# Kernel optimization log

Hardware: AMD Instinct MI355X
Metric: run time of the kernel (lower is better)

Reference implementation:

```python
import jax, jax.numpy as jnp
import numpy as np

N_NODES = 100000
N_EDGES = 1600000
IN_CH = 128
HIDDEN = 64
N_CLASSES = 40


def setup_inputs() -> dict:
    key = jax.random.key(0)
    k_x, k_e, k_w1, k_w2 = jax.random.split(key, 4)
    x = jax.random.normal(k_x, (N_NODES, IN_CH), dtype=jnp.float32)
    edge_index = jax.random.randint(k_e, (2, N_EDGES), 0, N_NODES, dtype=jnp.int64)
    # Glorot-style init for GCN weights
    W1 = jax.random.normal(k_w1, (IN_CH, HIDDEN), dtype=jnp.float32) * (1.0 / np.sqrt(IN_CH))
    b1 = jnp.zeros((HIDDEN,), dtype=jnp.float32)
    W2 = jax.random.normal(k_w2, (HIDDEN, N_CLASSES), dtype=jnp.float32) * (1.0 / np.sqrt(HIDDEN))
    b2 = jnp.zeros((N_CLASSES,), dtype=jnp.float32)
    return {"x": x, "edge_index": edge_index, "W1": W1, "b1": b1, "W2": W2, "b2": b2}


def reference(x, edge_index, W1, b1, W2, b2):
    n = x.shape[0]
    # PyG GCNConv: add self-loops, symmetric degree normalization
    loop = jnp.arange(n, dtype=edge_index.dtype)
    src = jnp.concatenate([edge_index[0], loop])  # message sources j
    dst = jnp.concatenate([edge_index[1], loop])  # aggregation targets i
    w = jnp.ones(src.shape[0], dtype=x.dtype)     # edge_weight=None -> ones
    deg = jax.ops.segment_sum(w, dst, num_segments=n)
    dinv = jnp.where(deg > 0, jax.lax.rsqrt(jnp.maximum(deg, 1e-12)), 0.0)
    norm = dinv[src] * dinv[dst]                  # [E+N]

    def gcn_conv(h, W, b):
        hw = h @ W                                # transform first (fewer flops)
        msg = hw[src] * norm[:, None]             # gather + normalize
        return jax.ops.segment_sum(msg, dst, num_segments=n) + b  # scatter-add

    h = jax.nn.relu(gcn_conv(x, W1, b1))
    # dropout is identity in eval mode
    out = gcn_conv(h, W2, b2)
    return out
```

## Files before the change

kernel.cpp:

```cpp
#include <hip/hip_runtime.h>
#include <hip/hip_bf16.h>

#define NNODES 100000
#define NEDGES 1600000
#define IN_CH 128
#define HID 64
#define NC 40
#define NPAD 100352
#define NBUK 196
#define CAP 9216
#define BCHUNK 4096
#define NBIN 391

typedef unsigned short ushort_t;
typedef unsigned int uint_t;
typedef __attribute__((ext_vector_type(8))) short short8;
typedef __attribute__((ext_vector_type(4))) float floatx4;

__device__ __forceinline__ ushort_t f2bf(float f) {
    union { float ff; unsigned int i; } t;
    t.ff = f;
    unsigned int r = t.i + 0x7fff + ((t.i >> 16) & 1);
    return (ushort_t)(r >> 16);
}
__device__ __forceinline__ float2 unpk(uint_t p) {
    union { unsigned int i; float f; } a, b;
    a.i = p << 16;
    b.i = p & 0xffff0000u;
    return make_float2(a.f, b.f);
}
__device__ __forceinline__ void acc2(float2& a, uint_t p) {
    union { unsigned int i; float f; } lo, hi;
    lo.i = p << 16;
    hi.i = p & 0xffff0000u;
    a.x += lo.f;
    a.y += hi.f;
}

__global__ __launch_bounds__(256) void k_init(
    const float* __restrict__ W1, ushort_t* __restrict__ Wp,
    int* __restrict__ gcur, ushort_t* __restrict__ hb, int n)
{
    int b = blockIdx.x, t = threadIdx.x;
    if (b < 32) {
        int i = b * 256 + t;
        int j = i & 7;
        int m = (i >> 3) & 15;
        int ct = (i >> 7) & 3;
        int quad = (i >> 9) & 3;
        int kc = i >> 11;
        int k = kc * 32 + quad * 8 + j;
        int c = ct * 16 + m;
        Wp[i] = f2bf(W1[k * HID + c]);
    } else {
        if (t < NBUK) gcur[t] = t * CAP;
        uint_t* hbz = (uint_t*)(hb + (size_t)n * HID);
        if (t >= 224) hbz[t - 224] = 0;
    }
}

__global__ __launch_bounds__(256) void k_bin0(
    const int* __restrict__ srcs, const int* __restrict__ dsts,
    int* __restrict__ gcur, uint_t* __restrict__ tmp, int e)
{
    __shared__ uint_t pk[BCHUNK];
    __shared__ ushort_t bk[BCHUNK];
    __shared__ int hist[NBUK];
    __shared__ int base[NBUK];
    int t = threadIdx.x;
    int begin = blockIdx.x * BCHUNK;
    int cnt = e - begin; if (cnt > BCHUNK) cnt = BCHUNK;

    for (int i = t; i < NBUK; i += 256) hist[i] = 0;
    __syncthreads();
    for (int j = t; j < cnt; j += 256) {
        int d = dsts[begin + j];
        int s = srcs[begin + j];
        int b = d >> 9;
        pk[j] = (uint_t)s | ((uint_t)(d & 511) << 17);
        bk[j] = (ushort_t)b;
        atomicAdd(&hist[b], 1);
    }
    __syncthreads();
    for (int i = t; i < NBUK; i += 256) {
        base[i] = atomicAdd(&gcur[i], hist[i]);
        hist[i] = 0;
    }
    __syncthreads();
    for (int j = t; j < cnt; j += 256) {
        int b = bk[j];
        int r = atomicAdd(&hist[b], 1);
        int pos = base[b] + r;
        if (pos < (b + 1) * CAP) tmp[pos] = pk[j];
    }
}

__global__ __launch_bounds__(256) void k_sort(
    const uint_t* __restrict__ tmp, const int* __restrict__ gcur,
    int* __restrict__ row_start, float* __restrict__ dinv,
    uint_t* __restrict__ es, int n, int e)
{
    __shared__ int cnt[512];
    __shared__ int sc[512];
    __shared__ int red[256];
    int t = threadIdx.x;
    int b = blockIdx.x;
    int d0 = b << 9;
    int total = gcur[b] - b * CAP;
    if (total > CAP) total = CAP;
    int part = 0;
    for (int i = t; i < b; i += 256) part += gcur[i] - i * CAP;
    red[t] = part;
    cnt[t] = 0; cnt[t + 256] = 0;
    __syncthreads();
    for (int off = 128; off > 0; off >>= 1) {
        if (t < off) red[t] += red[t + off];
        __syncthreads();
    }
    int gb = red[0];
    const uint_t* seg = tmp + b * CAP;
    for (int j = t; j < total; j += 256)
        atomicAdd(&cnt[seg[j] >> 17], 1);
    __syncthreads();
    sc[t] = cnt[t]; sc[t + 256] = cnt[t + 256];
    __syncthreads();
    for (int off = 1; off < 512; off <<= 1) {
        int v0 = (t >= off) ? sc[t - off] : 0;
        int i1 = t + 256;
        int v1 = (i1 >= off) ? sc[i1 - off] : 0;
        __syncthreads();
        sc[t] += v0; sc[i1] += v1;
        __syncthreads();
    }
#pragma unroll
    for (int q = 0; q < 2; ++q) {
        int i = t + q * 256;
        int node = d0 + i;
        int start = gb + sc[i] - cnt[i];
        if (node < n) {
            row_start[node] = start;
            dinv[node] = rsqrtf((float)cnt[i] + 1.0f);
        }
        cnt[i] = start;
    }
    __syncthreads();
    for (int j = t; j < total; j += 256) {
        uint_t p = seg[j];
        int ld = (int)(p >> 17);
        int pos = atomicAdd(&cnt[ld], 1);
        es[pos] = p & 0x1FFFFu;
    }
    if (b == NBUK - 1 && t == 0) row_start[n] = e;
}

__global__ __launch_bounds__(256) void k_gemm1(
    const float* __restrict__ x, const ushort_t* __restrict__ Wp,
    const float* __restrict__ dinv, ushort_t* __restrict__ hw1, int n)
{
    int wave = threadIdx.x >> 6;
    int lane = threadIdx.x & 63;
    int m = lane & 15;
    int quad = lane >> 4;
    int row = blockIdx.x * 64 + wave * 16 + m;
    int rowc = row < n ? row : (n - 1);
    const float* xr = x + (size_t)rowc * IN_CH + quad * 8;

    floatx4 acc[4];
#pragma unroll
    for (int ct = 0; ct < 4; ++ct) acc[ct] = (floatx4){0.f, 0.f, 0.f, 0.f};

#pragma unroll
    for (int kc = 0; kc < 4; ++kc) {
        float4 xa = *(const float4*)(xr + kc * 32);
        float4 xb = *(const float4*)(xr + kc * 32 + 4);
        short8 a;
        a[0] = (short)f2bf(xa.x); a[1] = (short)f2bf(xa.y);
        a[2] = (short)f2bf(xa.z); a[3] = (short)f2bf(xa.w);
        a[4] = (short)f2bf(xb.x); a[5] = (short)f2bf(xb.y);
        a[6] = (short)f2bf(xb.z); a[7] = (short)f2bf(xb.w);
#pragma unroll
        for (int ct = 0; ct < 4; ++ct) {
            short8 b = *(const short8*)(Wp + ((((kc * 4 + quad) * 4 + ct) * 16 + m) << 3));
            acc[ct] = __builtin_amdgcn_mfma_f32_16x16x32_bf16(a, b, acc[ct], 0, 0, 0);
        }
    }
    int r0 = blockIdx.x * 64 + wave * 16 + quad * 4;
#pragma unroll
    for (int r = 0; r < 4; ++r) {
        int rr = r0 + r;
        if (rr < n) {
            float di = dinv[rr];
            ushort_t* o = hw1 + (size_t)rr * HID + m;
#pragma unroll
            for (int ct = 0; ct < 4; ++ct) o[ct * 16] = f2bf(acc[ct][r] * di);
        } else if (rr == n) {
            ushort_t* o = hw1 + (size_t)n * HID + m;
#pragma unroll
            for (int ct = 0; ct < 4; ++ct) o[ct * 16] = 0;
        }
    }
}

__global__ __launch_bounds__(256) void k_agg1(
    const int* __restrict__ row_start, const uint_t* __restrict__ es,
    const float* __restrict__ dinv, const uint_t* __restrict__ hw1u,
    const float* __restrict__ b1, ushort_t* __restrict__ hb, int n)
{
    int lane = threadIdx.x & 63;
    int obase = lane & 56;
    int ol = lane & 7;
    int node = blockIdx.x * 32 + (threadIdx.x >> 3);
    bool valid = node < n;
    int rs = valid ? row_start[node] : 0;
    int re = valid ? row_start[node + 1] : 0;
    float di = valid ? dinv[node] : 0.f;
    int selfrow = valid ? node : n;

    float2 c0, c1, c2, c3;
    {
        uint4 sp = *(const uint4*)(hw1u + (size_t)selfrow * 32 + ol * 4);
        c0 = unpk(sp.x); c1 = unpk(sp.y); c2 = unpk(sp.z); c3 = unpk(sp.w);
    }
    for (int base = rs; base < re; base += 8) {
        int idx = base + ol;
        int el = (idx < re) ? (int)es[idx] : n;
        uint4 p[8];
#pragma unroll
        for (int b = 0; b < 8; ++b) {
            int s = __shfl(el, obase + b);
            p[b] = *(const uint4*)(hw1u + (size_t)s * 32 + ol * 4);
        }
#pragma unroll
        for (int b = 0; b < 8; ++b) {
            acc2(c0, p[b].x); acc2(c1, p[b].y);
            acc2(c2, p[b].z); acc2(c3, p[b].w);
        }
    }
    if (valid) {
        float4 bb0 = ((const float4*)b1)[ol * 2];
        float4 bb1 = ((const float4*)b1)[ol * 2 + 1];
        float h0 = fmaxf(c0.x * di + bb0.x, 0.f);
        float h1 = fmaxf(c0.y * di + bb0.y, 0.f);
        float h2 = fmaxf(c1.x * di + bb0.z, 0.f);
        float h3 = fmaxf(c1.y * di + bb0.w, 0.f);
        float h4 = fmaxf(c2.x * di + bb1.x, 0.f);
        float h5 = fmaxf(c2.y * di + bb1.y, 0.f);
        float h6 = fmaxf(c3.x * di + bb1.z, 0.f);
        float h7 = fmaxf(c3.y * di + bb1.w, 0.f);
        uint4 st;
        st.x = (uint_t)f2bf(h0 * di) | ((uint_t)f2bf(h1 * di) << 16);
        st.y = (uint_t)f2bf(h2 * di) | ((uint_t)f2bf(h3 * di) << 16);
        st.z = (uint_t)f2bf(h4 * di) | ((uint_t)f2bf(h5 * di) << 16);
        st.w = (uint_t)f2bf(h6 * di) | ((uint_t)f2bf(h7 * di) << 16);
        *(uint4*)(hb + (size_t)node * HID + ol * 8) = st;
    }
}

__global__ __launch_bounds__(256) void k_agg2(
    const int* __restrict__ row_start, const uint_t* __restrict__ es,
    const float* __restrict__ dinv, const uint_t* __restrict__ hbu,
    float* __restrict__ hagg, int n)
{
    int lane = threadIdx.x & 63;
    int obase = lane & 56;
    int ol = lane & 7;
    int node = blockIdx.x * 32 + (threadIdx.x >> 3);
    bool valid = node < n;
    int rs = valid ? row_start[node] : 0;
    int re = valid ? row_start[node + 1] : 0;
    float di = valid ? dinv[node] : 0.f;
    int selfrow = valid ? node : n;

    float2 c0, c1, c2, c3;
    {
        uint4 sp = *(const uint4*)(hbu + (size_t)selfrow * 32 + ol * 4);
        c0 = unpk(sp.x); c1 = unpk(sp.y); c2 = unpk(sp.z); c3 = unpk(sp.w);
    }
    for (int base = rs; base < re; base += 8) {
        int idx = base + ol;
        int el = (idx < re) ? (int)es[idx] : n;
        uint4 p[8];
#pragma unroll
        for (int b = 0; b < 8; ++b) {
            int s = __shfl(el, obase + b);
            p[b] = *(const uint4*)(hbu + (size_t)s * 32 + ol * 4);
        }
#pragma unroll
        for (int b = 0; b < 8; ++b) {
            acc2(c0, p[b].x); acc2(c1, p[b].y);
            acc2(c2, p[b].z); acc2(c3, p[b].w);
        }
    }
    if (valid) {
        float4 o0, o1;
        o0.x = c0.x * di; o0.y = c0.y * di; o0.z = c1.x * di; o0.w = c1.y * di;
        o1.x = c2.x * di; o1.y = c2.y * di; o1.z = c3.x * di; o1.w = c3.y * di;
        float* hr = hagg + (size_t)node * HID + ol * 8;
        *(float4*)hr = o0;
        *(float4*)(hr + 4) = o1;
    }
}

__global__ __launch_bounds__(256) void k_gemm2f(
    const float* __restrict__ hagg, const float* __restrict__ W2,
    const float* __restrict__ b2, float* __restrict__ out, int n)
{
    __shared__ float wsm[HID * NC];
    for (int i = threadIdx.x; i < HID * NC; i += 256) wsm[i] = W2[i];
    __syncthreads();
    int row = blockIdx.x * 256 + threadIdx.x;
    if (row >= n) return;
    const float4* hr = (const float4*)(hagg + (size_t)row * HID);
    float acc[NC];
#pragma unroll
    for (int c = 0; c < NC; ++c) acc[c] = b2[c];
#pragma unroll 4
    for (int k4 = 0; k4 < HID / 4; ++k4) {
        float4 hv = hr[k4];
        const float* w0 = wsm + (k4 * 4) * NC;
#pragma unroll
        for (int c = 0; c < NC; ++c)
            acc[c] += hv.x * w0[c] + hv.y * w0[c + NC] + hv.z * w0[c + 2 * NC] + hv.w * w0[c + 3 * NC];
    }
    float* o = out + (size_t)row * NC;
#pragma unroll
    for (int c4 = 0; c4 < NC / 4; ++c4) {
        float4 st = make_float4(acc[4 * c4], acc[4 * c4 + 1], acc[4 * c4 + 2], acc[4 * c4 + 3]);
        *(float4*)(o + 4 * c4) = st;
    }
}

extern "C" void kernel_launch(void* const* d_in, const int* in_sizes, int n_in,
                              void* d_out, int out_size, void* d_ws, size_t ws_size,
                              hipStream_t stream) {
    const float* x  = (const float*)d_in[0];
    const int* edge = (const int*)d_in[1];
    const float* W1 = (const float*)d_in[2];
    const float* b1 = (const float*)d_in[3];
    const float* W2 = (const float*)d_in[4];
    const float* b2 = (const float*)d_in[5];
    float* out      = (float*)d_out;

    const int n = in_sizes[0] / IN_CH;
    const int e = in_sizes[1] / 2;
    const int* srcs = edge;
    const int* dsts = edge + e;

    int*      gcur      = (int*)d_ws;
    int*      row_start = gcur + 256;
    float*    dinv      = (float*)(row_start + NPAD);
    uint_t*   tmp       = (uint_t*)(dinv + NPAD);
    uint_t*   es        = tmp + (size_t)NBUK * CAP;
    ushort_t* Wp        = (ushort_t*)(es + NEDGES);
    ushort_t* hw1       = Wp + 8192;
    ushort_t* hb        = hw1 + (size_t)(NNODES + 1) * HID;
    float*    hagg      = (float*)(hb + (size_t)(NNODES + 1) * HID);

    k_init<<<33, 256, 0, stream>>>(W1, Wp, gcur, hb, n);
    k_bin0<<<NBIN, 256, 0, stream>>>(srcs, dsts, gcur, tmp, e);
    k_sort<<<NBUK, 256, 0, stream>>>(tmp, gcur, row_start, dinv, es, n, e);
    k_gemm1<<<(n + 63) / 64, 256, 0, stream>>>(x, Wp, dinv, hw1, n);
    k_agg1<<<(n + 31) / 32, 256, 0, stream>>>(row_start, es, dinv, (const uint_t*)hw1, b1, hb, n);
    k_agg2<<<(n + 31) / 32, 256, 0, stream>>>(row_start, es, dinv, (const uint_t*)hb, hagg, n);
    k_gemm2f<<<(n + 255) / 256, 256, 0, stream>>>(hagg, W2, b2, out, n);
}
```

Before: 238.1 us.

## Fuse second GEMM into layer-2 aggregation and fold init into binning kernel

The layer-2 aggregation now keeps each block's 32 aggregated rows in shared memory and multiplies them by W2 (staged in LDS) directly, writing the final output. This removes the fp32 hagg intermediate round trip through global memory and one kernel launch. The init kernel is replaced by a memset of the bucket cursors plus an extra block in the binning kernel that packs W1 and zeroes the pad row. Bucket offsets are now added at use time. Accumulators switch to a 2-wide float vector type, which may allow packed adds. Each agg2 block now does extra LDS work and holds more shared memory, which may reduce occupancy.

```diff
diff --git a/kernel.cpp b/kernel.cpp
--- a/kernel.cpp
+++ b/kernel.cpp
@@ -16,6 +16,7 @@
 typedef unsigned int uint_t;
 typedef __attribute__((ext_vector_type(8))) short short8;
 typedef __attribute__((ext_vector_type(4))) float floatx4;
+typedef __attribute__((ext_vector_type(2))) float f32x2;
 
 __device__ __forceinline__ ushort_t f2bf(float f) {
     union { float ff; unsigned int i; } t;
@@ -23,51 +24,40 @@
     unsigned int r = t.i + 0x7fff + ((t.i >> 16) & 1);
     return (ushort_t)(r >> 16);
 }
-__device__ __forceinline__ float2 unpk(uint_t p) {
-    union { unsigned int i; float f; } a, b;
-    a.i = p << 16;
-    b.i = p & 0xffff0000u;
-    return make_float2(a.f, b.f);
-}
-__device__ __forceinline__ void acc2(float2& a, uint_t p) {
+__device__ __forceinline__ void acc2(f32x2& a, uint_t p) {
     union { unsigned int i; float f; } lo, hi;
     lo.i = p << 16;
     hi.i = p & 0xffff0000u;
-    a.x += lo.f;
-    a.y += hi.f;
-}
-
-__global__ __launch_bounds__(256) void k_init(
-    const float* __restrict__ W1, ushort_t* __restrict__ Wp,
-    int* __restrict__ gcur, ushort_t* __restrict__ hb, int n)
-{
-    int b = blockIdx.x, t = threadIdx.x;
-    if (b < 32) {
-        int i = b * 256 + t;
-        int j = i & 7;
-        int m = (i >> 3) & 15;
-        int ct = (i >> 7) & 3;
-        int quad = (i >> 9) & 3;
-        int kc = i >> 11;
-        int k = kc * 32 + quad * 8 + j;
-        int c = ct * 16 + m;
-        Wp[i] = f2bf(W1[k * HID + c]);
-    } else {
-        if (t < NBUK) gcur[t] = t * CAP;
-        uint_t* hbz = (uint_t*)(hb + (size_t)n * HID);
-        if (t >= 224) hbz[t - 224] = 0;
-    }
+    f32x2 v = {lo.f, hi.f};
+    a += v;
 }
 
 __global__ __launch_bounds__(256) void k_bin0(
     const int* __restrict__ srcs, const int* __restrict__ dsts,
-    int* __restrict__ gcur, uint_t* __restrict__ tmp, int e)
+    int* __restrict__ gcur, uint_t* __restrict__ tmp, int e,
+    const float* __restrict__ W1, ushort_t* __restrict__ Wp,
+    ushort_t* __restrict__ hb, int n)
 {
     __shared__ uint_t pk[BCHUNK];
     __shared__ ushort_t bk[BCHUNK];
     __shared__ int hist[NBUK];
     __shared__ int base[NBUK];
     int t = threadIdx.x;
+    if (blockIdx.x >= NBIN) {
+        for (int i = t; i < IN_CH * HID; i += 256) {
+            int j = i & 7;
+            int m = (i >> 3) & 15;
+            int ct = (i >> 7) & 3;
+            int quad = (i >> 9) & 3;
+            int kc = i >> 11;
+            int k = kc * 32 + quad * 8 + j;
+            int c = ct * 16 + m;
+            Wp[i] = f2bf(W1[k * HID + c]);
+        }
+        uint_t* hbz = (uint_t*)(hb + (size_t)n * HID);
+        if (t < 32) hbz[t] = 0;
+        return;
+    }
     int begin = blockIdx.x * BCHUNK;
     int cnt = e - begin; if (cnt > BCHUNK) cnt = BCHUNK;
 
@@ -83,7 +73,7 @@
     }
     __syncthreads();
     for (int i = t; i < NBUK; i += 256) {
-        base[i] = atomicAdd(&gcur[i], hist[i]);
+        base[i] = i * CAP + atomicAdd(&gcur[i], hist[i]);
         hist[i] = 0;
     }
     __syncthreads();
@@ -106,10 +96,10 @@
     int t = threadIdx.x;
     int b = blockIdx.x;
     int d0 = b << 9;
-    int total = gcur[b] - b * CAP;
+    int total = gcur[b];
     if (total > CAP) total = CAP;
     int part = 0;
-    for (int i = t; i < b; i += 256) part += gcur[i] - i * CAP;
+    for (int i = t; i < b; i += 256) part += gcur[i];
     red[t] = part;
     cnt[t] = 0; cnt[t + 256] = 0;
     __syncthreads();
@@ -216,10 +206,11 @@
     float di = valid ? dinv[node] : 0.f;
     int selfrow = valid ? node : n;
 
-    float2 c0, c1, c2, c3;
+    f32x2 c0, c1, c2, c3;
     {
         uint4 sp = *(const uint4*)(hw1u + (size_t)selfrow * 32 + ol * 4);
-        c0 = unpk(sp.x); c1 = unpk(sp.y); c2 = unpk(sp.z); c3 = unpk(sp.w);
+        c0 = (f32x2){0.f, 0.f}; c1 = c0; c2 = c0; c3 = c0;
+        acc2(c0, sp.x); acc2(c1, sp.y); acc2(c2, sp.z); acc2(c3, sp.w);
     }
     for (int base = rs; base < re; base += 8) {
         int idx = base + ol;
@@ -259,22 +250,30 @@
 __global__ __launch_bounds__(256) void k_agg2(
     const int* __restrict__ row_start, const uint_t* __restrict__ es,
     const float* __restrict__ dinv, const uint_t* __restrict__ hbu,
-    float* __restrict__ hagg, int n)
-{
+    const float* __restrict__ W2, const float* __restrict__ b2,
+    float* __restrict__ out, int n)
+{
+    __shared__ float wsm[HID * NC];
+    __shared__ float hsm[32][68];
+    for (int i = threadIdx.x; i < HID * NC; i += 256) wsm[i] = W2[i];
+    __syncthreads();
+
     int lane = threadIdx.x & 63;
     int obase = lane & 56;
     int ol = lane & 7;
-    int node = blockIdx.x * 32 + (threadIdx.x >> 3);
+    int slot = threadIdx.x >> 3;
+    int node = blockIdx.x * 32 + slot;
     bool valid = node < n;
     int rs = valid ? row_start[node] : 0;
     int re = valid ? row_start[node + 1] : 0;
     float di = valid ? dinv[node] : 0.f;
     int selfrow = valid ? node : n;
 
-    float2 c0, c1, c2, c3;
+    f32x2 c0, c1, c2, c3;
     {
         uint4 sp = *(const uint4*)(hbu + (size_t)selfrow * 32 + ol * 4);
-        c0 = unpk(sp.x); c1 = unpk(sp.y); c2 = unpk(sp.z); c3 = unpk(sp.w);
+        c0 = (f32x2){0.f, 0.f}; c1 = c0; c2 = c0; c3 = c0;
+        acc2(c0, sp.x); acc2(c1, sp.y); acc2(c2, sp.z); acc2(c3, sp.w);
     }
     for (int base = rs; base < re; base += 8) {
         int idx = base + ol;
@@ -291,42 +290,37 @@
             acc2(c2, p[b].z); acc2(c3, p[b].w);
         }
     }
-    if (valid) {
-        float4 o0, o1;
-        o0.x = c0.x * di; o0.y = c0.y * di; o0.z = c1.x * di; o0.w = c1.y * di;
-        o1.x = c2.x * di; o1.y = c2.y * di; o1.z = c3.x * di; o1.w = c3.y * di;
-        float* hr = hagg + (size_t)node * HID + ol * 8;
-        *(float4*)hr = o0;
-        *(float4*)(hr + 4) = o1;
-    }
-}
-
-__global__ __launch_bounds__(256) void k_gemm2f(
-    const float* __restrict__ hagg, const float* __restrict__ W2,
-    const float* __restrict__ b2, float* __restrict__ out, int n)
-{
-    __shared__ float wsm[HID * NC];
-    for (int i = threadIdx.x; i < HID * NC; i += 256) wsm[i] = W2[i];
-    __syncthreads();
-    int row = blockIdx.x * 256 + threadIdx.x;
-    if (row >= n) return;
-    const float4* hr = (const float4*)(hagg + (size_t)row * HID);
-    float acc[NC];
-#pragma unroll
-    for (int c = 0; c < NC; ++c) acc[c] = b2[c];
+    {
+        float4 g0, g1;
+        g0.x = c0.x * di; g0.y = c0.y * di; g0.z = c1.x * di; g0.w = c1.y * di;
+        g1.x = c2.x * di; g1.y = c2.y * di; g1.z = c3.x * di; g1.w = c3.y * di;
+        *(float4*)&hsm[slot][ol * 8] = g0;
+        *(float4*)&hsm[slot][ol * 8 + 4] = g1;
+    }
+    int w8 = (threadIdx.x >> 6) * 8;
+    int qm = lane >> 4;
+    int lq = lane & 15;
+    int lw = (lq < 10) ? lq : 0;
+    const float4* w4 = (const float4*)wsm;
+#pragma unroll
+    for (int pass = 0; pass < 2; ++pass) {
+        int slot2 = w8 + pass * 4 + qm;
+        int node2 = blockIdx.x * 32 + slot2;
+        float4 acc = ((const float4*)b2)[lw];
 #pragma unroll 4
-    for (int k4 = 0; k4 < HID / 4; ++k4) {
-        float4 hv = hr[k4];
-        const float* w0 = wsm + (k4 * 4) * NC;
-#pragma unroll
-        for (int c = 0; c < NC; ++c)
-            acc[c] += hv.x * w0[c] + hv.y * w0[c + NC] + hv.z * w0[c + 2 * NC] + hv.w * w0[c + 3 * NC];
-    }
-    float* o = out + (size_t)row * NC;
-#pragma unroll
-    for (int c4 = 0; c4 < NC / 4; ++c4) {
-        float4 st = make_float4(acc[4 * c4], acc[4 * c4 + 1], acc[4 * c4 + 2], acc[4 * c4 + 3]);
-        *(float4*)(o + 4 * c4) = st;
+        for (int k4 = 0; k4 < 16; ++k4) {
+            float4 hk = *(const float4*)&hsm[slot2][k4 * 4];
+            float4 w0 = w4[(k4 * 4 + 0) * 10 + lw];
+            float4 w1 = w4[(k4 * 4 + 1) * 10 + lw];
+            float4 w2 = w4[(k4 * 4 + 2) * 10 + lw];
+            float4 w3 = w4[(k4 * 4 + 3) * 10 + lw];
+            acc.x += hk.x * w0.x + hk.y * w1.x + hk.z * w2.x + hk.w * w3.x;
+            acc.y += hk.x * w0.y + hk.y * w1.y + hk.z * w2.y + hk.w * w3.y;
+            acc.z += hk.x * w0.z + hk.y * w1.z + hk.z * w2.z + hk.w * w3.z;
+            acc.w += hk.x * w0.w + hk.y * w1.w + hk.z * w2.w + hk.w * w3.w;
+        }
+        if (node2 < n && lq < 10)
+            *(float4*)(out + (size_t)node2 * NC + lq * 4) = acc;
     }
 }
 
@@ -354,13 +348,11 @@
     ushort_t* Wp        = (ushort_t*)(es + NEDGES);
     ushort_t* hw1       = Wp + 8192;
     ushort_t* hb        = hw1 + (size_t)(NNODES + 1) * HID;
-    float*    hagg      = (float*)(hb + (size_t)(NNODES + 1) * HID);
-
-    k_init<<<33, 256, 0, stream>>>(W1, Wp, gcur, hb, n);
-    k_bin0<<<NBIN, 256, 0, stream>>>(srcs, dsts, gcur, tmp, e);
+
+    hipMemsetAsync(gcur, 0, NBUK * sizeof(int), stream);
+    k_bin0<<<NBIN + 1, 256, 0, stream>>>(srcs, dsts, gcur, tmp, e, W1, Wp, hb, n);
     k_sort<<<NBUK, 256, 0, stream>>>(tmp, gcur, row_start, dinv, es, n, e);
     k_gemm1<<<(n + 63) / 64, 256, 0, stream>>>(x, Wp, dinv, hw1, n);
     k_agg1<<<(n + 31) / 32, 256, 0, stream>>>(row_start, es, dinv, (const uint_t*)hw1, b1, hb, n);
-    k_agg2<<<(n + 31) / 32, 256, 0, stream>>>(row_start, es, dinv, (const uint_t*)hb, hagg, n);
-    k_gemm2f<<<(n + 255) / 256, 256, 0, stream>>>(hagg, W2, b2, out, n);
-}
+    k_agg2<<<(n + 31) / 32, 256, 0, stream>>>(row_start, es, dinv, (const uint_t*)hb, W2, b2, out, n);
+}
```

Result: faster. 220.8 us (-7.3%).
